# Optimization experiments

Hardware: AMD Instinct MI355X
Metric: run time of the kernel (lower is better)

## Reference

```python
import jax, jax.numpy as jnp
import numpy as np

WS = 8  # window size (hardcoded in original forward)

def _window_partition(x, ws=WS):
    b, c, h, w = x.shape
    ph = (-h) % ws
    pw = (-w) % ws
    x = jnp.pad(x, ((0, 0), (0, 0), (0, ph), (0, pw)), mode='reflect')
    H, W = h + ph, w + pw
    # matches torch .view(b,c,ws,H//ws,ws,W//ws).permute(0,1,2,4,3,5)
    x = x.reshape(b, c, ws, H // ws, ws, W // ws)
    x = x.transpose(0, 1, 2, 4, 3, 5).reshape(b, c * ws * ws, H // ws, W // ws)
    return x, h, w, c, H // ws

def _l2norm_dim1(x):
    # F.normalize(x, p=2) defaults to dim=1 (token axis for [b, L, d]), eps=1e-12
    n = jnp.sqrt(jnp.sum(x * x, axis=1, keepdims=True))
    return x / jnp.maximum(n, 1e-12)

def _forward(q, k, v):
    b = q.shape[0]
    qp, qh, qw, qc, patch = _window_partition(q)
    kp, _, _, _, _ = _window_partition(k)
    vp, _, _, _, _ = _window_partition(v)
    d = qp.shape[1]  # c * ws * ws
    qt = qp.transpose(0, 2, 3, 1).reshape(b, -1, d)  # [b, L, d]
    kt = kp.transpose(0, 2, 3, 1).reshape(b, -1, d)
    vt = vp.transpose(0, 2, 3, 1).reshape(b, -1, d)
    _q = _l2norm_dim1(qt)
    _k = _l2norm_dim1(kt)
    _v = _l2norm_dim1(vt)
    sim = jnp.einsum('bld,bmd->blm', _q, _k) * (d ** -0.5)  # [b, L, L]
    out = jnp.einsum('blm,bmd->bld', jax.nn.softmax(sim, axis=-1), _v)
    # window_reverse
    L = out.shape[1]
    ws = WS
    x = out.reshape(b, patch, L // patch, qc, ws, ws)
    x = x.transpose(0, 3, 4, 1, 5, 2)  # (b, c, ws, patch, ws, L//patch)
    H = ws * patch
    x = x.reshape(b, qc, H, -1)
    return x[:, :, :qh, :qw]

def setup_inputs() -> dict:
    key = jax.random.key(0)
    kq, kk, kv = jax.random.split(key, 3)
    shape = (8, 32, 252, 252)
    return {
        'q': jax.random.normal(kq, shape, dtype=jnp.float32),
        'k': jax.random.normal(kk, shape, dtype=jnp.float32),
        'v': jax.random.normal(kv, shape, dtype=jnp.float32),
    }

def reference(q, k, v):
    return _forward(q, k, v)
```

## Files before the change

### kernel.cpp

```cpp
#include <hip/hip_runtime.h>
#include <cstdint>
#include <cstddef>


typedef __bf16 bf16x8 __attribute__((ext_vector_type(8)));
typedef float  f32x4  __attribute__((ext_vector_type(4)));

__device__ __forceinline__ unsigned int f2bf(float f) {
  unsigned int u = __builtin_bit_cast(unsigned int, f);
  u += 0x7FFFu + ((u >> 16) & 1u);
  return u >> 16;
}
__device__ __forceinline__ float bf2f(unsigned short h) {
  return __builtin_bit_cast(float, (unsigned int)h << 16);
}

__device__ __forceinline__ void load_lds16(const void* g, void* l) {
  __builtin_amdgcn_global_load_lds(
      (const __attribute__((address_space(1))) void*)g,
      (__attribute__((address_space(3))) void*)l, 16, 0, 0);
}

__global__ void norm_kernel(const float* __restrict__ q,
                            const float* __restrict__ k,
                            const float* __restrict__ v,
                            float* __restrict__ scales) {
  int bx = blockIdx.x;
  int t   = bx >> 11;
  int rem = bx & 2047;
  int b   = rem >> 8;
  int c   = (rem >> 3) & 31;
  int i0  = rem & 7;
  const float* x = (t == 0) ? q : (t == 1) ? k : v;
  const float* base = x + ((size_t)b * 32 + c) * 63504;

  int tid   = threadIdx.x;
  int chunk = tid & 63;
  int i1b   = tid >> 6;

  float cw0 = 1.f, cw1 = 1.f, cw2 = 1.f, cw3 = 1.f;
  bool skipc = false;
  if (chunk == 61) cw3 = 2.f;
  else if (chunk == 62) { cw0 = cw1 = cw2 = 2.f; }
  else if (chunk == 63) skipc = true;

  float s = 0.f;
  if (!skipc) {
    #pragma unroll
    for (int r = 0; r < 8; r++) {
      int i1 = r * 4 + i1b;
      int h  = i0 * 32 + i1;
      if (h < 252) {
        float rw = (i0 == 7 && h >= 247 && h <= 250) ? 2.f : 1.f;
        float4 vv = *(const float4*)&base[(size_t)h * 252 + chunk * 4];
        s += rw * (cw0 * vv.x * vv.x + cw1 * vv.y * vv.y +
                   cw2 * vv.z * vv.z + cw3 * vv.w * vv.w);
      }
    }
  }
  __shared__ float red[256];
  red[tid] = s;
  __syncthreads();
  if (tid < 8) {
    float acc = 0.f;
    #pragma unroll
    for (int w = 0; w < 4; w++)
      #pragma unroll
      for (int e = 0; e < 8; e++) acc += red[w * 64 + tid * 8 + e];
    float sc = 1.0f / fmaxf(sqrtf(acc), 1e-12f);
    scales[((size_t)(t * 8 + b)) * 2048 + i0 * 256 + tid * 32 + c] = sc;
  }
}

__global__ void pack_kernel(const float* __restrict__ q,
                            const float* __restrict__ k,
                            const float* __restrict__ v,
                            const float* __restrict__ scales,
                            unsigned short* __restrict__ Qh,
                            unsigned short* __restrict__ Kh,
                            unsigned short* __restrict__ Vt) {
  int bx = blockIdx.x;
  int t   = bx >> 11;
  int rem = bx & 2047;
  int b   = rem >> 8;
  int i0  = (rem >> 5) & 7;
  int i1  = rem & 31;
  const float* x = (t == 0) ? q : (t == 1) ? k : v;

  __shared__ unsigned short tile[32 * 256];
  __shared__ float scl[256];

  int tid = threadIdx.x;
  scl[tid] = scales[((size_t)(t * 8 + b)) * 2048 + i0 * 256 + tid];
  __syncthreads();

  int h  = i0 * 32 + i1;
  int hs = (h < 252) ? h : 502 - h;
  const float* xb = x + (size_t)b * 32 * 63504 + (size_t)hs * 252;

  #pragma unroll
  for (int r = 0; r < 8; r++) {
    int idx   = r * 256 + tid;
    int c     = idx >> 6;
    int chunk = idx & 63;
    const float* src = xb + (size_t)c * 63504;
    if (chunk < 63) {
      float sc = scl[(chunk >> 3) * 32 + c];
      float4 vv = *(const float4*)&src[chunk * 4];
      uint2 o;
      o.x = f2bf(vv.x * sc) | (f2bf(vv.y * sc) << 16);
      o.y = f2bf(vv.z * sc) | (f2bf(vv.w * sc) << 16);
      *(uint2*)&tile[c * 256 + chunk * 4] = o;
    } else {
      float sc = scl[7 * 32 + c];
      float a0 = src[250], a1 = src[249], a2 = src[248], a3 = src[247];
      uint2 o;
      o.x = f2bf(a0 * sc) | (f2bf(a1 * sc) << 16);
      o.y = f2bf(a2 * sc) | (f2bf(a3 * sc) << 16);
      *(uint2*)&tile[c * 256 + 252] = o;
    }
  }
  __syncthreads();

  if (t < 2) {
    unsigned short* X = ((t == 0) ? Qh : Kh) + (size_t)b * 1024 * 2048;
    #pragma unroll
    for (int r = 0; r < 4; r++) {
      int g  = r * 2048 + tid * 8;
      int j1 = g >> 8;
      int p0 = g & 255;
      int j0w = p0 >> 5;
      int c0  = p0 & 31;
      unsigned int ov[4];
      #pragma unroll
      for (int m = 0; m < 4; m++) {
        unsigned int lo = tile[(c0 + 2 * m)     * 256 + j0w * 32 + j1];
        unsigned int hi = tile[(c0 + 2 * m + 1) * 256 + j0w * 32 + j1];
        ov[m] = lo | (hi << 16);
      }
      int l = i1 * 32 + j1;
      uint4 o4; o4.x = ov[0]; o4.y = ov[1]; o4.z = ov[2]; o4.w = ov[3];
      *(uint4*)&X[(size_t)l * 2048 + i0 * 256 + p0] = o4;
    }
  } else {
    unsigned short* V = Vt + (size_t)b * 2048 * 1024;
    int rrow = tid;
    int c   = rrow & 31;
    int j0r = rrow >> 5;
    unsigned short* dst = &V[(size_t)(i0 * 256 + rrow) * 1024 + i1 * 32];
    const unsigned short* src = &tile[c * 256 + j0r * 32];
    #pragma unroll
    for (int m = 0; m < 4; m++) {
      *(uint4*)&dst[m * 8] = *(const uint4*)&src[m * 8];
    }
  }
}

template <int MODE>
__global__ __launch_bounds__(256, 4)
void gemm_nt(const unsigned short* __restrict__ A,
             const unsigned short* __restrict__ B,
             int K, int Asb, int Bsb, void* __restrict__ Cout, float scale) {
  __shared__ unsigned short lA[128 * 64];
  __shared__ unsigned short lB[128 * 64];

  const int tid  = threadIdx.x;
  const int lane = tid & 63;
  const int wave = tid >> 6;
  const int ln15 = lane & 15;
  const int q4   = lane >> 4;
  const int wm   = wave >> 1;
  const int wn   = wave & 1;
  const int m0   = blockIdx.y * 128;
  const int n0   = blockIdx.x * 128;
  const unsigned short* Ab = A + (size_t)blockIdx.z * Asb;
  const unsigned short* Bb = B + (size_t)blockIdx.z * Bsb;

  const int srow = lane >> 3;
  const int kcp  = lane & 7;
  const int kcl  = kcp ^ srow;

  f32x4 acc[4][4] = {};

  for (int k0 = 0; k0 < K; k0 += 64) {
    #pragma unroll
    for (int r = 0; r < 4; r++) {
      int rowg = wave * 32 + r * 8;
      int row  = rowg + srow;
      load_lds16(&Ab[(size_t)(m0 + row) * K + k0 + kcl * 8], &lA[rowg * 64]);
      load_lds16(&Bb[(size_t)(n0 + row) * K + k0 + kcl * 8], &lB[rowg * 64]);
    }
    __syncthreads();
    #pragma unroll
    for (int kk = 0; kk < 2; kk++) {
      bf16x8 af[4], bfr[4];
      #pragma unroll
      for (int mt = 0; mt < 4; mt++) {
        int row = wm * 64 + mt * 16 + ln15;
        int pc  = (kk * 4 + q4) ^ (row & 7);
        af[mt] = *(const bf16x8*)&lA[row * 64 + pc * 8];
      }
      #pragma unroll
      for (int nt = 0; nt < 4; nt++) {
        int row = wn * 64 + nt * 16 + ln15;
        int pc  = (kk * 4 + q4) ^ (row & 7);
        bfr[nt] = *(const bf16x8*)&lB[row * 64 + pc * 8];
      }
      #pragma unroll
      for (int mt = 0; mt < 4; mt++)
        #pragma unroll
        for (int nt = 0; nt < 4; nt++)
          acc[mt][nt] = __builtin_amdgcn_mfma_f32_16x16x32_bf16(
              af[mt], bfr[nt], acc[mt][nt], 0, 0, 0);
    }
    __syncthreads();
  }

  if (MODE == 0) {
    unsigned short* Sb = (unsigned short*)Cout + (size_t)blockIdx.z * 1024 * 1024;
    #pragma unroll
    for (int mt = 0; mt < 4; mt++) {
      #pragma unroll
      for (int nt = 0; nt < 4; nt++) {
        int col = n0 + wn * 64 + nt * 16 + ln15;
        #pragma unroll
        for (int rg = 0; rg < 4; rg++) {
          int rowi = m0 + wm * 64 + mt * 16 + q4 * 4 + rg;
          Sb[(size_t)rowi * 1024 + col] = (unsigned short)f2bf(acc[mt][nt][rg] * scale);
        }
      }
    }
  } else {
    float* Ob = (float*)Cout;
    int bb = blockIdx.z;
    #pragma unroll
    for (int mt = 0; mt < 4; mt++) {
      #pragma unroll
      for (int nt = 0; nt < 4; nt++) {
        int l  = n0 + wn * 64 + nt * 16 + ln15;
        int i1 = l >> 5, j1 = l & 31;
        #pragma unroll
        for (int rg = 0; rg < 4; rg++) {
          int dp = m0 + wm * 64 + mt * 16 + q4 * 4 + rg;
          int c  = dp & 31;
          int j0 = (dp >> 5) & 7;
          int i0 = dp >> 8;
          int h = i0 * 32 + i1;
          int w = j0 * 32 + j1;
          if (h < 252 && w < 252)
            Ob[(((size_t)bb * 32 + c) * 252 + h) * 252 + w] = acc[mt][nt][rg];
        }
      }
    }
  }
}

__global__ void softmax_kernel(unsigned short* __restrict__ S) {
  unsigned short* row = S + (size_t)blockIdx.x * 1024;
  int tid  = threadIdx.x;
  int lane = tid & 63;
  int wid  = tid >> 6;

  uint2 u = *(const uint2*)&row[tid * 4];
  float x0 = bf2f((unsigned short)(u.x & 0xFFFF));
  float x1 = bf2f((unsigned short)(u.x >> 16));
  float x2 = bf2f((unsigned short)(u.y & 0xFFFF));
  float x3 = bf2f((unsigned short)(u.y >> 16));

  __shared__ float red[8];
  float mx = fmaxf(fmaxf(x0, x1), fmaxf(x2, x3));
  #pragma unroll
  for (int off = 32; off > 0; off >>= 1) mx = fmaxf(mx, __shfl_down(mx, off));
  if (lane == 0) red[wid] = mx;
  __syncthreads();
  if (tid == 0)
    red[4] = fmaxf(fmaxf(red[0], red[1]), fmaxf(red[2], red[3]));
  __syncthreads();
  float bm = red[4];

  float e0 = __expf(x0 - bm), e1 = __expf(x1 - bm);
  float e2 = __expf(x2 - bm), e3 = __expf(x3 - bm);
  float s = e0 + e1 + e2 + e3;
  #pragma unroll
  for (int off = 32; off > 0; off >>= 1) s += __shfl_down(s, off);
  if (lane == 0) red[wid] = s;
  __syncthreads();
  if (tid == 0) red[5] = 1.0f / (red[0] + red[1] + red[2] + red[3]);
  __syncthreads();
  float inv = red[5];

  unsigned int o0 = f2bf(e0 * inv) | (f2bf(e1 * inv) << 16);
  unsigned int o1 = f2bf(e2 * inv) | (f2bf(e3 * inv) << 16);
  uint2 o; o.x = o0; o.y = o1;
  *(uint2*)&row[tid * 4] = o;
}

extern "C" void kernel_launch(void* const* d_in, const int* in_sizes, int n_in,
                              void* d_out, int out_size, void* d_ws, size_t ws_size,
                              hipStream_t stream) {
  const float* q = (const float*)d_in[0];
  const float* k = (const float*)d_in[1];
  const float* v = (const float*)d_in[2];
  float* out = (float*)d_out;

  char* ws = (char*)d_ws;
  float* scales = (float*)ws;
  unsigned short* Qh = (unsigned short*)(ws + 196608);
  unsigned short* Kh = Qh + (size_t)8 * 1024 * 2048;
  unsigned short* Vt = Kh + (size_t)8 * 1024 * 2048;
  unsigned short* S  = Vt + (size_t)8 * 2048 * 1024;

  const float SIM_SCALE = 0.02209708691207961f;

  norm_kernel<<<6144, 256, 0, stream>>>(q, k, v, scales);
  pack_kernel<<<6144, 256, 0, stream>>>(q, k, v, scales, Qh, Kh, Vt);
  gemm_nt<0><<<dim3(8, 8, 8), 256, 0, stream>>>(
      Qh, Kh, 2048, 1024 * 2048, 1024 * 2048, (void*)S, SIM_SCALE);
  softmax_kernel<<<8192, 256, 0, stream>>>(S);
  gemm_nt<1><<<dim3(8, 16, 8), 256, 0, stream>>>(
      Vt, S, 1024, 2048 * 1024, 1024 * 1024, (void*)out, 1.0f);
}
```

Measured before the change: 392.0 us.

## Split Q/K and V packing, fold V normalization into output GEMM epilogue

Rewrites norm_kernel so each block reduces 64 rows of one channel with per-column coalesced loads, giving fewer and larger blocks. The combined pack kernel is split into a Q/K pack that uses a padded, rotated float LDS tile to avoid bank conflicts during the transpose, and a separate V pack that reads directly from global memory without LDS. V is packed unnormalized, and its per-row L2 scale is applied in the second GEMM's epilogue, since scaling the d dimension commutes with the attention matmul. This removes a dependency and some LDS traffic, but adds a scale load and a multiply to the GEMM store path and changes bf16 rounding slightly.

```diff
diff --git a/kernel.cpp b/kernel.cpp
--- a/kernel.cpp
+++ b/kernel.cpp
@@ -26,73 +26,70 @@
                             const float* __restrict__ v,
                             float* __restrict__ scales) {
   int bx = blockIdx.x;
-  int t   = bx >> 11;
-  int rem = bx & 2047;
-  int b   = rem >> 8;
-  int c   = (rem >> 3) & 31;
-  int i0  = rem & 7;
+  int t = bx >> 10;
+  int b = (bx >> 7) & 7;
+  int c = (bx >> 2) & 31;
+  int g = bx & 3;
   const float* x = (t == 0) ? q : (t == 1) ? k : v;
   const float* base = x + ((size_t)b * 32 + c) * 63504;
 
-  int tid   = threadIdx.x;
-  int chunk = tid & 63;
-  int i1b   = tid >> 6;
-
-  float cw0 = 1.f, cw1 = 1.f, cw2 = 1.f, cw3 = 1.f;
-  bool skipc = false;
-  if (chunk == 61) cw3 = 2.f;
-  else if (chunk == 62) { cw0 = cw1 = cw2 = 2.f; }
-  else if (chunk == 63) skipc = true;
-
-  float s = 0.f;
-  if (!skipc) {
-    #pragma unroll
-    for (int r = 0; r < 8; r++) {
-      int i1 = r * 4 + i1b;
-      int h  = i0 * 32 + i1;
-      if (h < 252) {
-        float rw = (i0 == 7 && h >= 247 && h <= 250) ? 2.f : 1.f;
-        float4 vv = *(const float4*)&base[(size_t)h * 252 + chunk * 4];
-        s += rw * (cw0 * vv.x * vv.x + cw1 * vv.y * vv.y +
-                   cw2 * vv.z * vv.z + cw3 * vv.w * vv.w);
-      }
-    }
-  }
-  __shared__ float red[256];
-  red[tid] = s;
-  __syncthreads();
-  if (tid < 8) {
-    float acc = 0.f;
-    #pragma unroll
-    for (int w = 0; w < 4; w++)
-      #pragma unroll
-      for (int e = 0; e < 8; e++) acc += red[w * 64 + tid * 8 + e];
-    float sc = 1.0f / fmaxf(sqrtf(acc), 1e-12f);
-    scales[((size_t)(t * 8 + b)) * 2048 + i0 * 256 + tid * 32 + c] = sc;
-  }
-}
-
-__global__ void pack_kernel(const float* __restrict__ q,
-                            const float* __restrict__ k,
-                            const float* __restrict__ v,
-                            const float* __restrict__ scales,
-                            unsigned short* __restrict__ Qh,
-                            unsigned short* __restrict__ Kh,
-                            unsigned short* __restrict__ Vt) {
+  int tid = threadIdx.x;
+  int w = tid;
+  bool active = (w < 252);
+  float cw = ((unsigned)(w - 247) <= 3u) ? 2.f : 1.f;
+
+  float acc0 = 0.f, acc1 = 0.f;
+  if (active) {
+    int h0 = g * 64;
+    int nrows = (g == 3) ? 60 : 64;
+    #pragma unroll 8
+    for (int hh = 0; hh < 64; hh++) {
+      if (hh < nrows) {
+        int h = h0 + hh;
+        float val = base[(size_t)h * 252 + w];
+        float v2 = val * val;
+        if ((unsigned)(h - 247) <= 3u) v2 *= 2.f;
+        if (hh < 32) acc0 += v2; else acc1 += v2;
+      }
+    }
+  }
+  acc0 *= cw; acc1 *= cw;
+
+  __shared__ float red[512];
+  red[tid] = acc0;
+  red[256 + tid] = acc1;
+  __syncthreads();
+  if (tid < 16) {
+    int i0loc = tid >> 3;
+    int j0    = tid & 7;
+    float s = 0.f;
+    #pragma unroll
+    for (int e = 0; e < 32; e++) s += red[i0loc * 256 + j0 * 32 + e];
+    float sc = 1.0f / fmaxf(sqrtf(s), 1e-12f);
+    int i0 = g * 2 + i0loc;
+    scales[((size_t)(t * 8 + b)) * 2048 + i0 * 256 + j0 * 32 + c] = sc;
+  }
+}
+
+__global__ void pack_qk_kernel(const float* __restrict__ q,
+                               const float* __restrict__ k,
+                               const float* __restrict__ scales,
+                               unsigned short* __restrict__ Qh,
+                               unsigned short* __restrict__ Kh) {
   int bx = blockIdx.x;
   int t   = bx >> 11;
   int rem = bx & 2047;
   int b   = rem >> 8;
   int i0  = (rem >> 5) & 7;
   int i1  = rem & 31;
-  const float* x = (t == 0) ? q : (t == 1) ? k : v;
-
-  __shared__ unsigned short tile[32 * 256];
-  __shared__ float scl[256];
+  const float* x = (t == 0) ? q : k;
+
+  __shared__ float tf[32 * 257];
+  __shared__ float sclt[256];
 
   int tid = threadIdx.x;
-  scl[tid] = scales[((size_t)(t * 8 + b)) * 2048 + i0 * 256 + tid];
-  __syncthreads();
+  sclt[(tid & 31) * 8 + (tid >> 5)] =
+      scales[((size_t)(t * 8 + b)) * 2048 + i0 * 256 + tid];
 
   int h  = i0 * 32 + i1;
   int hs = (h < 252) ? h : 502 - h;
@@ -100,59 +97,90 @@
 
   #pragma unroll
   for (int r = 0; r < 8; r++) {
-    int idx   = r * 256 + tid;
-    int c     = idx >> 6;
-    int chunk = idx & 63;
+    int c     = r * 4 + (tid >> 6);
+    int chunk = tid & 63;
     const float* src = xb + (size_t)c * 63504;
+    int j0 = chunk >> 3, cq = chunk & 7;
+    float4 vv;
     if (chunk < 63) {
-      float sc = scl[(chunk >> 3) * 32 + c];
-      float4 vv = *(const float4*)&src[chunk * 4];
-      uint2 o;
-      o.x = f2bf(vv.x * sc) | (f2bf(vv.y * sc) << 16);
-      o.y = f2bf(vv.z * sc) | (f2bf(vv.w * sc) << 16);
-      *(uint2*)&tile[c * 256 + chunk * 4] = o;
+      vv = *(const float4*)&src[chunk * 4];
     } else {
-      float sc = scl[7 * 32 + c];
-      float a0 = src[250], a1 = src[249], a2 = src[248], a3 = src[247];
-      uint2 o;
-      o.x = f2bf(a0 * sc) | (f2bf(a1 * sc) << 16);
-      o.y = f2bf(a2 * sc) | (f2bf(a3 * sc) << 16);
-      *(uint2*)&tile[c * 256 + 252] = o;
-    }
-  }
-  __syncthreads();
-
-  if (t < 2) {
-    unsigned short* X = ((t == 0) ? Qh : Kh) + (size_t)b * 1024 * 2048;
-    #pragma unroll
-    for (int r = 0; r < 4; r++) {
-      int g  = r * 2048 + tid * 8;
-      int j1 = g >> 8;
-      int p0 = g & 255;
-      int j0w = p0 >> 5;
-      int c0  = p0 & 31;
-      unsigned int ov[4];
-      #pragma unroll
-      for (int m = 0; m < 4; m++) {
-        unsigned int lo = tile[(c0 + 2 * m)     * 256 + j0w * 32 + j1];
-        unsigned int hi = tile[(c0 + 2 * m + 1) * 256 + j0w * 32 + j1];
-        ov[m] = lo | (hi << 16);
-      }
-      int l = i1 * 32 + j1;
-      uint4 o4; o4.x = ov[0]; o4.y = ov[1]; o4.z = ov[2]; o4.w = ov[3];
-      *(uint4*)&X[(size_t)l * 2048 + i0 * 256 + p0] = o4;
-    }
-  } else {
-    unsigned short* V = Vt + (size_t)b * 2048 * 1024;
-    int rrow = tid;
-    int c   = rrow & 31;
-    int j0r = rrow >> 5;
-    unsigned short* dst = &V[(size_t)(i0 * 256 + rrow) * 1024 + i1 * 32];
-    const unsigned short* src = &tile[c * 256 + j0r * 32];
+      vv.x = src[250]; vv.y = src[249]; vv.z = src[248]; vv.w = src[247];
+    }
+    float* row = &tf[c * 257 + j0 * 32];
+    int p = cq * 4 + j0;
+    row[p & 31]       = vv.x;
+    row[(p + 1) & 31] = vv.y;
+    row[(p + 2) & 31] = vv.z;
+    row[(p + 3) & 31] = vv.w;
+  }
+  __syncthreads();
+
+  int p0  = (tid * 8) & 255;
+  int j0w = p0 >> 5;
+  int c0  = p0 & 31;
+  float scl_r[8];
+  #pragma unroll
+  for (int m = 0; m < 8; m++) scl_r[m] = sclt[(c0 + m) * 8 + j0w];
+
+  unsigned short* X = ((t == 0) ? Qh : Kh) + (size_t)b * 1024 * 2048;
+  #pragma unroll
+  for (int r = 0; r < 4; r++) {
+    int j1 = r * 8 + (tid >> 5);
+    int rot = (j1 + j0w) & 31;
+    unsigned int ov[4];
     #pragma unroll
     for (int m = 0; m < 4; m++) {
-      *(uint4*)&dst[m * 8] = *(const uint4*)&src[m * 8];
-    }
+      float lo = tf[(c0 + 2 * m)     * 257 + j0w * 32 + rot] * scl_r[2 * m];
+      float hi = tf[(c0 + 2 * m + 1) * 257 + j0w * 32 + rot] * scl_r[2 * m + 1];
+      ov[m] = f2bf(lo) | (f2bf(hi) << 16);
+    }
+    int l = i1 * 32 + j1;
+    uint4 o4; o4.x = ov[0]; o4.y = ov[1]; o4.z = ov[2]; o4.w = ov[3];
+    *(uint4*)&X[(size_t)l * 2048 + i0 * 256 + p0] = o4;
+  }
+}
+
+__global__ void pack_v_kernel(const float* __restrict__ v,
+                              unsigned short* __restrict__ Vt) {
+  int bx = blockIdx.x;
+  int b  = bx >> 8;
+  int i0 = (bx >> 5) & 7;
+  int i1 = bx & 31;
+  int h  = i0 * 32 + i1;
+  int hs = (h < 252) ? h : 502 - h;
+  const float* src = v + (size_t)b * 32 * 63504 + (size_t)hs * 252;
+  unsigned short* dst = Vt + (size_t)b * 2048 * 1024
+                           + (size_t)(i0 * 256) * 1024 + i1 * 32;
+
+  int tid = threadIdx.x;
+  int j1c = tid & 3;
+  int c   = (tid >> 2) & 31;
+  int j0g = tid >> 7;
+  const float* s = src + (size_t)c * 63504;
+
+  #pragma unroll
+  for (int jj = 0; jj < 4; jj++) {
+    int j0 = j0g * 4 + jj;
+    int w0 = j0 * 32 + j1c * 8;
+    float f0, f1, f2, f3, f4, f5, f6, f7;
+    if (w0 + 8 <= 252) {
+      float4 a = *(const float4*)&s[w0];
+      float4 bq = *(const float4*)&s[w0 + 4];
+      f0 = a.x; f1 = a.y; f2 = a.z; f3 = a.w;
+      f4 = bq.x; f5 = bq.y; f6 = bq.z; f7 = bq.w;
+    } else {
+      float4 a = *(const float4*)&s[244];
+      float4 bq = *(const float4*)&s[248];
+      f0 = bq.x; f1 = bq.y; f2 = bq.z; f3 = bq.w;
+      f4 = bq.z; f5 = bq.y; f6 = bq.x; f7 = a.w;
+    }
+    uint4 o;
+    o.x = f2bf(f0) | (f2bf(f1) << 16);
+    o.y = f2bf(f2) | (f2bf(f3) << 16);
+    o.z = f2bf(f4) | (f2bf(f5) << 16);
+    o.w = f2bf(f6) | (f2bf(f7) << 16);
+    *(uint4*)&dst[(size_t)(j0 * 32 + c) * 1024 + j1c * 8] = o;
   }
 }
 
@@ -160,9 +188,11 @@
 __global__ __launch_bounds__(256, 4)
 void gemm_nt(const unsigned short* __restrict__ A,
              const unsigned short* __restrict__ B,
-             int K, int Asb, int Bsb, void* __restrict__ Cout, float scale) {
+             int K, int Asb, int Bsb, void* __restrict__ Cout, float scale,
+             const float* __restrict__ sv) {
   __shared__ unsigned short lA[128 * 64];
   __shared__ unsigned short lB[128 * 64];
+  __shared__ float svb[(MODE == 1) ? 128 : 1];
 
   const int tid  = threadIdx.x;
   const int lane = tid & 63;
@@ -176,6 +206,9 @@
   const unsigned short* Ab = A + (size_t)blockIdx.z * Asb;
   const unsigned short* Bb = B + (size_t)blockIdx.z * Bsb;
 
+  if (MODE == 1 && tid < 128)
+    svb[tid] = sv[(size_t)blockIdx.z * 2048 + m0 + tid];
+
   const int srow = lane >> 3;
   const int kcp  = lane & 7;
   const int kcl  = kcp ^ srow;
@@ -241,14 +274,16 @@
         int i1 = l >> 5, j1 = l & 31;
         #pragma unroll
         for (int rg = 0; rg < 4; rg++) {
-          int dp = m0 + wm * 64 + mt * 16 + q4 * 4 + rg;
+          int rloc = wm * 64 + mt * 16 + q4 * 4 + rg;
+          int dp = m0 + rloc;
           int c  = dp & 31;
           int j0 = (dp >> 5) & 7;
           int i0 = dp >> 8;
           int h = i0 * 32 + i1;
           int w = j0 * 32 + j1;
           if (h < 252 && w < 252)
-            Ob[(((size_t)bb * 32 + c) * 252 + h) * 252 + w] = acc[mt][nt][rg];
+            Ob[(((size_t)bb * 32 + c) * 252 + h) * 252 + w] =
+                acc[mt][nt][rg] * svb[rloc];
         }
       }
     }
@@ -311,12 +346,14 @@
   unsigned short* S  = Vt + (size_t)8 * 2048 * 1024;
 
   const float SIM_SCALE = 0.02209708691207961f;
-
-  norm_kernel<<<6144, 256, 0, stream>>>(q, k, v, scales);
-  pack_kernel<<<6144, 256, 0, stream>>>(q, k, v, scales, Qh, Kh, Vt);
+  const float* sv = scales + (size_t)2 * 8 * 2048;
+
+  norm_kernel<<<3072, 256, 0, stream>>>(q, k, v, scales);
+  pack_qk_kernel<<<4096, 256, 0, stream>>>(q, k, scales, Qh, Kh);
+  pack_v_kernel<<<2048, 256, 0, stream>>>(v, Vt);
   gemm_nt<0><<<dim3(8, 8, 8), 256, 0, stream>>>(
-      Qh, Kh, 2048, 1024 * 2048, 1024 * 2048, (void*)S, SIM_SCALE);
+      Qh, Kh, 2048, 1024 * 2048, 1024 * 2048, (void*)S, SIM_SCALE, nullptr);
   softmax_kernel<<<8192, 256, 0, stream>>>(S);
   gemm_nt<1><<<dim3(8, 16, 8), 256, 0, stream>>>(
-      Vt, S, 1024, 2048 * 1024, 1024 * 1024, (void*)out, 1.0f);
-}
+      Vt, S, 1024, 2048 * 1024, 1024 * 1024, (void*)out, 1.0f, sv);
+}
```

Measured after the change: 426.2 us. 1.09x slower.
